# Performance work log

Measured on AMD Instinct MI355X. Metric: run time of the kernel, lower is better.

## Reference

```python
import jax, jax.numpy as jnp
import numpy as np

NUM_BLOCKS = 8
BLOCK_SIZE = 96
HIDDEN_FACTOR = 1
B, H, W = 1, 360, 181


def setup_inputs() -> dict:
    key = jax.random.key(0)
    k_inp, k_w, k_b = jax.random.split(key, 3)
    out_size = BLOCK_SIZE * HIDDEN_FACTOR
    inp = jax.random.normal(k_inp, (B, NUM_BLOCKS, BLOCK_SIZE, H, W, 2), dtype=jnp.float32)
    weight = jax.random.normal(k_w, (NUM_BLOCKS, BLOCK_SIZE, out_size, 2), dtype=jnp.float32) * 0.02
    bias = jax.random.normal(k_b, (NUM_BLOCKS, out_size, 1, 1, 2), dtype=jnp.float32) * 0.02
    return {"inp": inp, "weight": weight, "bias": bias}


def reference(inp, weight, bias):
    # inp:    [b, k, i, x, y, 2]  (last dim = real/imag)
    # weight: [k, i, o, 2]; bias: [k, o, 1, 1, 2]
    ar, ai = inp[..., 0], inp[..., 1]
    wr, wi = weight[..., 0], weight[..., 1]
    # complex matmul: (ar + i*ai) @ (wr + i*wi), block-diagonal over k
    real = jnp.einsum("bkixy,kio->bkoxy", ar, wr) - jnp.einsum("bkixy,kio->bkoxy", ai, wi)
    imag = jnp.einsum("bkixy,kio->bkoxy", ai, wr) + jnp.einsum("bkixy,kio->bkoxy", ar, wi)
    return jnp.stack([real, imag], axis=-1) + bias  # [b, k, o, x, y, 2]
```

## Files before the change

kernel.cpp:

```cpp
#include <hip/hip_runtime.h>

#define XY 65160
#define NI 96
#define NO 96
#define NK 8
#define NT2 510

typedef __attribute__((ext_vector_type(8))) short short8;
typedef __attribute__((ext_vector_type(4))) float floatx4;

union FragU { short8 v; unsigned u[4]; };

static __device__ __forceinline__ unsigned bf16r(float x) {
    unsigned u = __builtin_bit_cast(unsigned, x);
    return (u + 0x7FFFu + ((u >> 16) & 1u)) >> 16;
}
static __device__ __forceinline__ unsigned pk_bf16(float lo, float hi) {
    return bf16r(lo) | (bf16r(hi) << 16);
}

__global__ __launch_bounds__(256) void cmult_kernel(
    const float* __restrict__ inp, const float* __restrict__ weight,
    const float* __restrict__ bias, float* __restrict__ out)
{
    __shared__ unsigned wlds[36 * 64 * 4];
    __shared__ float2 blds[NO];

    const int tid  = threadIdx.x;
    const int lane = tid & 63;
    const int wave = tid >> 6;
    const int k    = blockIdx.y;
    const int l15  = lane & 15;
    const int quad = lane >> 4;

    const float* wk   = weight + (size_t)k * NI * NO * 2;
    const float* inpk = inp    + (size_t)k * NI * XY * 2;

    for (int idx = tid; idx < NI * NO; idx += 256) {
        int i = idx / NO;
        int o = idx - i * NO;
        float2 w = *reinterpret_cast<const float2*>(wk + (size_t)idx * 2);
        int s = i >> 4, q = (i >> 2) & 3, t = i & 3;
        int m = o >> 4, c = o & 15;
        wlds[((s * 6 + m) * 64 + (q * 16 + c)) * 4 + t] = pk_bf16(w.x, w.y);
    }
    if (tid < NO) {
        blds[tid] = *reinterpret_cast<const float2*>(bias + ((size_t)k * NO + tid) * 2);
    }
    __syncthreads();

    for (int tidx = blockIdx.x; tidx < NT2; tidx += gridDim.x) {
        int x0  = tidx * 128 + wave * 32 + 2 * l15;
        int x0c = x0 <= XY - 2 ? x0 : XY - 2;

        floatx4 accRA[6], accIA[6], accRB[6], accIB[6];
        #pragma unroll
        for (int m = 0; m < 6; ++m) {
            accRA[m] = (floatx4){0.f,0.f,0.f,0.f}; accIA[m] = (floatx4){0.f,0.f,0.f,0.f};
            accRB[m] = (floatx4){0.f,0.f,0.f,0.f}; accIB[m] = (floatx4){0.f,0.f,0.f,0.f};
        }

        #pragma unroll
        for (int s = 0; s < 6; ++s) {
            FragU bfrA, bfrB;
            #pragma unroll
            for (int t = 0; t < 4; ++t) {
                int i = 16 * s + 4 * quad + t;
                float4 a = *reinterpret_cast<const float4*>(inpk + ((size_t)i * XY + x0c) * 2);
                bfrA.u[t] = pk_bf16(a.x, a.y);
                bfrB.u[t] = pk_bf16(a.z, a.w);
            }
            #pragma unroll
            for (int m = 0; m < 6; ++m) {
                uint4 wp = *(reinterpret_cast<const uint4*>(wlds) + (s * 6 + m) * 64 + lane);
                unsigned pw[4] = {wp.x, wp.y, wp.z, wp.w};
                FragU w0, w1;
                #pragma unroll
                for (int t = 0; t < 4; ++t) {
                    w0.u[t] = pw[t] ^ 0x80000000u;
                    w1.u[t] = (pw[t] >> 16) | (pw[t] << 16);
                }
                accRA[m] = __builtin_amdgcn_mfma_f32_16x16x32_bf16(w0.v, bfrA.v, accRA[m], 0, 0, 0);
                accIA[m] = __builtin_amdgcn_mfma_f32_16x16x32_bf16(w1.v, bfrA.v, accIA[m], 0, 0, 0);
                accRB[m] = __builtin_amdgcn_mfma_f32_16x16x32_bf16(w0.v, bfrB.v, accRB[m], 0, 0, 0);
                accIB[m] = __builtin_amdgcn_mfma_f32_16x16x32_bf16(w1.v, bfrB.v, accIB[m], 0, 0, 0);
            }
        }

        if (x0 < XY) {
            #pragma unroll
            for (int m = 0; m < 6; ++m) {
                #pragma unroll
                for (int r = 0; r < 4; ++r) {
                    int o = 16 * m + 4 * quad + r;
                    float2 b = blds[o];
                    float4 ov;
                    ov.x = accRA[m][r] + b.x;
                    ov.y = accIA[m][r] + b.y;
                    ov.z = accRB[m][r] + b.x;
                    ov.w = accIB[m][r] + b.y;
                    *reinterpret_cast<float4*>(out + ((size_t)(k * NO + o) * XY + x0) * 2) = ov;
                }
            }
        }
    }
}

extern "C" void kernel_launch(void* const* d_in, const int* in_sizes, int n_in,
                              void* d_out, int out_size, void* d_ws, size_t ws_size,
                              hipStream_t stream)
{
    const float* inp    = (const float*)d_in[0];
    const float* weight = (const float*)d_in[1];
    const float* bias   = (const float*)d_in[2];
    float* out = (float*)d_out;

    dim3 grid(128, NK), block(256);
    hipLaunchKernelGGL(cmult_kernel, grid, block, 0, stream, inp, weight, bias, out);
}
```

Before: 731.5 us.

## Split output channels across wave pairs and use hardware bf16 pack conversion

Doubles the block to 512 threads and has each pair of waves split the six output-channel tiles, so each wave holds half the accumulators and occupancy can rise. The input fragment is loaded redundantly by both waves of a pair. The negate and swap for the complex product now apply to the input fragments once per k-step instead of to the weights for every tile. Software bf16 rounding is replaced with the v_cvt_pk_bf16_f32 instruction. The trade is doubled global input loads, hopefully served from cache, in exchange for lower register pressure.

```diff
diff --git a/kernel.cpp b/kernel.cpp
--- a/kernel.cpp
+++ b/kernel.cpp
@@ -11,15 +11,13 @@
 
 union FragU { short8 v; unsigned u[4]; };
 
-static __device__ __forceinline__ unsigned bf16r(float x) {
-    unsigned u = __builtin_bit_cast(unsigned, x);
-    return (u + 0x7FFFu + ((u >> 16) & 1u)) >> 16;
-}
-static __device__ __forceinline__ unsigned pk_bf16(float lo, float hi) {
-    return bf16r(lo) | (bf16r(hi) << 16);
+static __device__ __forceinline__ unsigned cvt_pk(float lo, float hi) {
+    unsigned r;
+    asm("v_cvt_pk_bf16_f32 %0, %1, %2" : "=v"(r) : "v"(lo), "v"(hi));
+    return r;
 }
 
-__global__ __launch_bounds__(256) void cmult_kernel(
+__global__ __launch_bounds__(512, 4) void cmult_kernel(
     const float* __restrict__ inp, const float* __restrict__ weight,
     const float* __restrict__ bias, float* __restrict__ out)
 {
@@ -29,6 +27,8 @@
     const int tid  = threadIdx.x;
     const int lane = tid & 63;
     const int wave = tid >> 6;
+    const int h    = wave & 1;
+    const int g    = wave >> 1;
     const int k    = blockIdx.y;
     const int l15  = lane & 15;
     const int quad = lane >> 4;
@@ -36,13 +36,13 @@
     const float* wk   = weight + (size_t)k * NI * NO * 2;
     const float* inpk = inp    + (size_t)k * NI * XY * 2;
 
-    for (int idx = tid; idx < NI * NO; idx += 256) {
+    for (int idx = tid; idx < NI * NO; idx += 512) {
         int i = idx / NO;
         int o = idx - i * NO;
         float2 w = *reinterpret_cast<const float2*>(wk + (size_t)idx * 2);
         int s = i >> 4, q = (i >> 2) & 3, t = i & 3;
         int m = o >> 4, c = o & 15;
-        wlds[((s * 6 + m) * 64 + (q * 16 + c)) * 4 + t] = pk_bf16(w.x, w.y);
+        wlds[((s * 6 + m) * 64 + (q * 16 + c)) * 4 + t] = cvt_pk(w.x, w.y);
     }
     if (tid < NO) {
         blds[tid] = *reinterpret_cast<const float2*>(bias + ((size_t)k * NO + tid) * 2);
@@ -50,55 +50,55 @@
     __syncthreads();
 
     for (int tidx = blockIdx.x; tidx < NT2; tidx += gridDim.x) {
-        int x0  = tidx * 128 + wave * 32 + 2 * l15;
+        int x0  = tidx * 128 + g * 32 + 2 * l15;
         int x0c = x0 <= XY - 2 ? x0 : XY - 2;
 
-        floatx4 accRA[6], accIA[6], accRB[6], accIB[6];
+        floatx4 accRA[3], accIA[3], accRB[3], accIB[3];
         #pragma unroll
-        for (int m = 0; m < 6; ++m) {
+        for (int m = 0; m < 3; ++m) {
             accRA[m] = (floatx4){0.f,0.f,0.f,0.f}; accIA[m] = (floatx4){0.f,0.f,0.f,0.f};
             accRB[m] = (floatx4){0.f,0.f,0.f,0.f}; accIB[m] = (floatx4){0.f,0.f,0.f,0.f};
         }
 
         #pragma unroll
         for (int s = 0; s < 6; ++s) {
-            FragU bfrA, bfrB;
+            FragU bNA, bSA, bNB, bSB;
             #pragma unroll
             for (int t = 0; t < 4; ++t) {
                 int i = 16 * s + 4 * quad + t;
                 float4 a = *reinterpret_cast<const float4*>(inpk + ((size_t)i * XY + x0c) * 2);
-                bfrA.u[t] = pk_bf16(a.x, a.y);
-                bfrB.u[t] = pk_bf16(a.z, a.w);
+                unsigned pA = cvt_pk(a.x, a.y);
+                unsigned pB = cvt_pk(a.z, a.w);
+                bNA.u[t] = pA ^ 0x80000000u;
+                bSA.u[t] = (pA >> 16) | (pA << 16);
+                bNB.u[t] = pB ^ 0x80000000u;
+                bSB.u[t] = (pB >> 16) | (pB << 16);
             }
             #pragma unroll
-            for (int m = 0; m < 6; ++m) {
+            for (int mm = 0; mm < 3; ++mm) {
+                int m = 3 * h + mm;
+                FragU wf;
                 uint4 wp = *(reinterpret_cast<const uint4*>(wlds) + (s * 6 + m) * 64 + lane);
-                unsigned pw[4] = {wp.x, wp.y, wp.z, wp.w};
-                FragU w0, w1;
-                #pragma unroll
-                for (int t = 0; t < 4; ++t) {
-                    w0.u[t] = pw[t] ^ 0x80000000u;
-                    w1.u[t] = (pw[t] >> 16) | (pw[t] << 16);
-                }
-                accRA[m] = __builtin_amdgcn_mfma_f32_16x16x32_bf16(w0.v, bfrA.v, accRA[m], 0, 0, 0);
-                accIA[m] = __builtin_amdgcn_mfma_f32_16x16x32_bf16(w1.v, bfrA.v, accIA[m], 0, 0, 0);
-                accRB[m] = __builtin_amdgcn_mfma_f32_16x16x32_bf16(w0.v, bfrB.v, accRB[m], 0, 0, 0);
-                accIB[m] = __builtin_amdgcn_mfma_f32_16x16x32_bf16(w1.v, bfrB.v, accIB[m], 0, 0, 0);
+                wf.u[0] = wp.x; wf.u[1] = wp.y; wf.u[2] = wp.z; wf.u[3] = wp.w;
+                accRA[mm] = __builtin_amdgcn_mfma_f32_16x16x32_bf16(wf.v, bNA.v, accRA[mm], 0, 0, 0);
+                accIA[mm] = __builtin_amdgcn_mfma_f32_16x16x32_bf16(wf.v, bSA.v, accIA[mm], 0, 0, 0);
+                accRB[mm] = __builtin_amdgcn_mfma_f32_16x16x32_bf16(wf.v, bNB.v, accRB[mm], 0, 0, 0);
+                accIB[mm] = __builtin_amdgcn_mfma_f32_16x16x32_bf16(wf.v, bSB.v, accIB[mm], 0, 0, 0);
             }
         }
 
         if (x0 < XY) {
             #pragma unroll
-            for (int m = 0; m < 6; ++m) {
+            for (int mm = 0; mm < 3; ++mm) {
                 #pragma unroll
                 for (int r = 0; r < 4; ++r) {
-                    int o = 16 * m + 4 * quad + r;
+                    int o = 16 * (3 * h + mm) + 4 * quad + r;
                     float2 b = blds[o];
                     float4 ov;
-                    ov.x = accRA[m][r] + b.x;
-                    ov.y = accIA[m][r] + b.y;
-                    ov.z = accRB[m][r] + b.x;
-                    ov.w = accIB[m][r] + b.y;
+                    ov.x = accRA[mm][r] + b.x;
+                    ov.y = accIA[mm][r] + b.y;
+                    ov.z = accRB[mm][r] + b.x;
+                    ov.w = accIB[mm][r] + b.y;
                     *reinterpret_cast<float4*>(out + ((size_t)(k * NO + o) * XY + x0) * 2) = ov;
                 }
             }
@@ -115,6 +115,6 @@
     const float* bias   = (const float*)d_in[2];
     float* out = (float*)d_out;
 
-    dim3 grid(128, NK), block(256);
+    dim3 grid(128, NK), block(512);
     hipLaunchKernelGGL(cmult_kernel, grid, block, 0, stream, inp, weight, bias, out);
 }
```

New measurement: 809.7 us. 1.11x slower.
